# Kernel optimization log

Measured on AMD Instinct MI355X. Metric: run time of the kernel, lower is better.

Reference implementation:

```python
import jax, jax.numpy as jnp
import numpy as np

EMBED_DIM = 1024
NUM_HEADS = 16
HEAD_DIM = EMBED_DIM // NUM_HEADS


def setup_inputs() -> dict:
    key = jax.random.key(0)
    ks = jax.random.split(key, 9)
    bs, seq_len = 4, 2048
    s = 1.0 / np.sqrt(EMBED_DIM)
    return {
        "x": jax.random.normal(ks[0], (bs, seq_len, EMBED_DIM), jnp.float32),
        "wq": jax.random.uniform(ks[1], (EMBED_DIM, EMBED_DIM), jnp.float32, -s, s),
        "bq": jax.random.uniform(ks[2], (EMBED_DIM,), jnp.float32, -s, s),
        "wk": jax.random.uniform(ks[3], (EMBED_DIM, EMBED_DIM), jnp.float32, -s, s),
        "bk": jax.random.uniform(ks[4], (EMBED_DIM,), jnp.float32, -s, s),
        "wv": jax.random.uniform(ks[5], (EMBED_DIM, EMBED_DIM), jnp.float32, -s, s),
        "bv": jax.random.uniform(ks[6], (EMBED_DIM,), jnp.float32, -s, s),
        "wo": jax.random.uniform(ks[7], (EMBED_DIM, EMBED_DIM), jnp.float32, -s, s),
        "bo": jax.random.uniform(ks[8], (EMBED_DIM,), jnp.float32, -s, s),
    }


def reference(x, wq, bq, wk, bk, wv, bv, wo, bo):
    bs, seq_len, _ = x.shape
    # projections (torch Linear: y = x @ W.T + b; here w stored as [out,in])
    q = x @ wq.T + bq
    k = x @ wk.T + bk
    v = x @ wv.T + bv
    # split heads -> (bs, heads, seq, head_dim)
    def split(t):
        return t.reshape(bs, seq_len, NUM_HEADS, HEAD_DIM).transpose(0, 2, 1, 3)
    q, k, v = split(q), split(k), split(v)
    scale = 1.0 / jnp.sqrt(jnp.asarray(HEAD_DIM, jnp.float32))
    scores = jnp.einsum("bhqd,bhkd->bhqk", q, k) * scale
    attn = jax.nn.softmax(scores, axis=-1)
    out = jnp.einsum("bhqk,bhkd->bhqd", attn, v)
    out = out.transpose(0, 2, 1, 3).reshape(bs, seq_len, EMBED_DIM)
    return out @ wo.T + bo
```

## Files before the change

kernel.cpp:

```cpp
#include <hip/hip_runtime.h>
#include <stdint.h>

#define SEQ 2048
#define BSZ 4
#define NH 16
#define HD 64
#define EMB 1024
#define NT (SEQ / 64)
#define QSCALE 0.1803368801111f

using bf16x8 = __attribute__((ext_vector_type(8))) __bf16;
using u16x8  = __attribute__((ext_vector_type(8))) unsigned short;
using u32x4  = __attribute__((ext_vector_type(4))) uint32_t;
using f32x4  = __attribute__((ext_vector_type(4))) float;
using f32x16 = __attribute__((ext_vector_type(16))) float;

__device__ __forceinline__ float exp2v(float x) { return __builtin_amdgcn_exp2f(x); }

__device__ __forceinline__ unsigned short f2bf(float f) {
    union { float f; uint32_t u; } v; v.f = f;
    uint32_t r = v.u + 0x7fffu + ((v.u >> 16) & 1u);
    return (unsigned short)(r >> 16);
}

__device__ __forceinline__ uint32_t cvtpk(float lo, float hi) {
    uint32_t r;
    asm("v_cvt_pk_bf16_f32 %0, %1, %2" : "=v"(r) : "v"(lo), "v"(hi));
    return r;
}
__device__ __forceinline__ void plswap(uint32_t& a, uint32_t& b) {
    asm volatile("v_permlane32_swap_b32 %0, %1" : "+v"(a), "+v"(b));
}

__device__ __forceinline__ void gload16(void* lds, const void* g) {
    __builtin_amdgcn_global_load_lds(
        (const __attribute__((address_space(1))) void*)g,
        (__attribute__((address_space(3))) void*)lds, 16, 0, 0);
}

__global__ void cast_kernel(const float* __restrict__ s, unsigned short* __restrict__ d, int n) {
    int i = (blockIdx.x * blockDim.x + threadIdx.x) * 4;
    if (i + 3 >= n) {
        for (int j = 0; j < 4 && i + j < n; ++j) d[i + j] = f2bf(s[i + j]);
        return;
    }
    float4 v = *(const float4*)(s + i);
    ushort4 o;
    o.x = f2bf(v.x); o.y = f2bf(v.y); o.z = f2bf(v.z); o.w = f2bf(v.w);
    *(ushort4*)(d + i) = o;
}

template <int MODE>
__global__ __launch_bounds__(256, 2)
void gemm_bt(const unsigned short* __restrict__ A,
             const unsigned short* __restrict__ Bw,
             const float* __restrict__ b0, const float* __restrict__ b1,
             const float* __restrict__ b2,
             void* __restrict__ C0, void* __restrict__ C1, void* __restrict__ C2,
             int M, int N, int Kd) {
    __shared__ unsigned short As[128][64];
    __shared__ unsigned short Bs[128][64];

    const int t    = threadIdx.x;
    const int lane = t & 63;
    const int wid  = t >> 6;
    const int g    = lane >> 4;
    const int lr   = lane & 15;
    const int wm   = wid >> 1, wn = wid & 1;
    const int m0   = blockIdx.x * 128, n0 = blockIdx.y * 128;
    const int srow = lane >> 3;
    const int scol = (lane & 7) * 8;

    f32x4 acc[4][4];
    const f32x4 zero = {0.f, 0.f, 0.f, 0.f};
#pragma unroll
    for (int i = 0; i < 4; ++i)
#pragma unroll
        for (int j = 0; j < 4; ++j) acc[i][j] = zero;

    for (int kt = 0; kt < Kd; kt += 64) {
#pragma unroll
        for (int p = 0; p < 4; ++p) {
            int rowA = wid * 32 + p * 8;
            gload16(&As[rowA][0], A  + (size_t)(m0 + rowA + srow) * Kd + kt + scol);
            gload16(&Bs[rowA][0], Bw + (size_t)(n0 + rowA + srow) * Kd + kt + scol);
        }
        __syncthreads();
#pragma unroll
        for (int ks = 0; ks < 2; ++ks) {
            bf16x8 af[4], bfr[4];
#pragma unroll
            for (int m = 0; m < 4; ++m)
                af[m] = *(const bf16x8*)&As[wm * 64 + m * 16 + lr][ks * 32 + g * 8];
#pragma unroll
            for (int n = 0; n < 4; ++n)
                bfr[n] = *(const bf16x8*)&Bs[wn * 64 + n * 16 + lr][ks * 32 + g * 8];
#pragma unroll
            for (int m = 0; m < 4; ++m)
#pragma unroll
                for (int n = 0; n < 4; ++n)
                    acc[m][n] = __builtin_amdgcn_mfma_f32_16x16x32_bf16(af[m], bfr[n], acc[m][n], 0, 0, 0);
        }
        __syncthreads();
    }

    const float* bias;
    unsigned short* Cw = nullptr;
    float* Cf = nullptr;
    float scl = 1.0f;
    int nl;
    if (MODE == 2) {
        int seg = n0 >> 10;
        bias = seg == 0 ? b0 : (seg == 1 ? b1 : b2);
        Cw = (unsigned short*)(seg == 0 ? C0 : (seg == 1 ? C1 : C2));
        scl = seg == 0 ? QSCALE : 1.0f;
        nl = n0 & 1023;
    } else {
        bias = b0; Cf = (float*)C0; nl = n0;
    }
#pragma unroll
    for (int n = 0; n < 4; ++n) {
        int colL = nl + wn * 64 + n * 16 + lr;
        float bv = bias[colL];
#pragma unroll
        for (int m = 0; m < 4; ++m) {
            int rowg = m0 + wm * 64 + m * 16 + g * 4;
#pragma unroll
            for (int r = 0; r < 4; ++r) {
                float val = (acc[m][n][r] + bv) * scl;
                if (MODE == 2)
                    Cw[(size_t)(rowg + r) * EMB + colL] = f2bf(val);
                else
                    Cf[(size_t)(rowg + r) * EMB + colL] = val;
            }
        }
    }
}

template <int M>
__device__ __forceinline__ void xr(uint32_t d[4], int i) {
    uint32_t o[4];
#pragma unroll
    for (int k = 0; k < 4; ++k) o[k] = (uint32_t)__shfl_xor((int)d[k], M);
    if (M == 1) {
        bool hi = (i & 1) != 0;
#pragma unroll
        for (int k = 0; k < 4; ++k)
            d[k] = hi ? ((d[k] & 0xffff0000u) | (o[k] >> 16))
                      : ((d[k] & 0x0000ffffu) | (o[k] << 16));
    } else {
        const int mb = M >> 1;
        bool hi = (i & M) != 0;
#pragma unroll
        for (int jd = 0; jd < 4; ++jd) {
            bool jdhi = (jd & mb) != 0;
            d[jd] = (jdhi != hi) ? o[jd ^ mb] : d[jd];
        }
    }
}

__global__ __launch_bounds__(256, 2)
void flash_attn(const unsigned short* __restrict__ Q,
                const unsigned short* __restrict__ K,
                const unsigned short* __restrict__ V,
                unsigned short* __restrict__ O) {
    __shared__ unsigned char KsB[2][64 * 128];
    __shared__ unsigned char VtB[2][64 * 128];

    const int t    = threadIdx.x;
    const int wid  = t >> 6;
    const int lane = t & 63;
    const int l31  = lane & 31;
    const int hi   = lane >> 5;
    const int hi16 = hi << 4;
    const int sw   = (l31 & 7) << 4;
    const int il   = lane & 7;
    const int b    = blockIdx.z, h = blockIdx.y;
    const int qbase = blockIdx.x * 128 + wid * 32;
    const size_t rowbase = (size_t)b * SEQ;
    const unsigned short* Kh = K + rowbase * EMB + h * HD;
    const unsigned short* Vh = V + rowbase * EMB + h * HD;

    bf16x8 qf[4];
#pragma unroll
    for (int db = 0; db < 4; ++db)
        qf[db] = *(const bf16x8*)(Q + (rowbase + qbase + l31) * EMB + h * HD + db * 16 + hi * 8);

    f32x16 o0, o1;
#pragma unroll
    for (int r = 0; r < 16; ++r) { o0[r] = 0.f; o1[r] = 0.f; }
    float me = -1e30f, lsum = 0.f;

    u16x8 kreg[2], vreg[2];
    auto load_tile = [&](int kt) {
#pragma unroll
        for (int p = 0; p < 2; ++p) {
            int c = p * 256 + t;
            kreg[p] = *(const u16x8*)(Kh + (size_t)(kt * 64 + (c >> 3)) * EMB + ((c & 7) << 3));
        }
#pragma unroll
        for (int vq = 0; vq < 2; ++vq)
            vreg[vq] = *(const u16x8*)(Vh + (size_t)(kt * 64 + (vq * 4 + wid) * 8 + il) * EMB
                                          + (((lane >> 3) & 7) << 3));
    };
    load_tile(0);

    for (int kt = 0; kt < NT; ++kt) {
        unsigned char* Ks = KsB[kt & 1];
        unsigned char* Vt = VtB[kt & 1];

        uint32_t tv[2][4];
#pragma unroll
        for (int vq = 0; vq < 2; ++vq) {
            u32x4 w = __builtin_bit_cast(u32x4, vreg[vq]);
#pragma unroll
            for (int k = 0; k < 4; ++k) tv[vq][k] = w[k];
            xr<4>(tv[vq], il);
            xr<2>(tv[vq], il);
            xr<1>(tv[vq], il);
        }
#pragma unroll
        for (int p = 0; p < 2; ++p) {
            int c = p * 256 + t;
            int row = c >> 3;
            *(u16x8*)(Ks + row * 128 + ((((c & 7) << 4)) ^ ((row & 7) << 4))) = kreg[p];
        }
#pragma unroll
        for (int vq = 0; vq < 2; ++vq)
            *(u32x4*)(Vt + lane * 128 + ((((vq * 4 + wid) << 4)) ^ ((lane & 7) << 4))) = *(u32x4*)tv[vq];

        if (kt + 1 < NT) load_tile(kt + 1);

        __syncthreads();

        f32x16 s0, s1;
#pragma unroll
        for (int r = 0; r < 16; ++r) { s0[r] = 0.f; s1[r] = 0.f; }
        __builtin_amdgcn_s_setprio(1);
#pragma unroll
        for (int db = 0; db < 4; ++db) {
            bf16x8 kf0 = *(const bf16x8*)(Ks + l31 * 128        + ((db * 32 + hi16) ^ sw));
            bf16x8 kf1 = *(const bf16x8*)(Ks + (l31 + 32) * 128 + ((db * 32 + hi16) ^ sw));
            s0 = __builtin_amdgcn_mfma_f32_32x32x16_bf16(kf0, qf[db], s0, 0, 0, 0);
            s1 = __builtin_amdgcn_mfma_f32_32x32x16_bf16(kf1, qf[db], s1, 0, 0, 0);
        }
        __builtin_amdgcn_s_setprio(0);

        float pm = fmaxf(s0[0], s0[1]);
#pragma unroll
        for (int r = 2; r < 16; ++r) pm = fmaxf(pm, s0[r]);
#pragma unroll
        for (int r = 0; r < 16; ++r) pm = fmaxf(pm, s1[r]);
        pm = fmaxf(pm, __shfl_xor(pm, 32));

        if (!__all(pm - me <= 8.0f)) {
            float mn = fmaxf(me, pm);
            float al = exp2v(me - mn);
            me = mn;
            lsum *= al;
#pragma unroll
            for (int r = 0; r < 16; ++r) {
                int addr = hi16 + (((r & 3) + 8 * (r >> 2)) << 2);
                float ar = __int_as_float(
                    __builtin_amdgcn_ds_bpermute(addr, __float_as_int(al)));
                o0[r] *= ar; o1[r] *= ar;
            }
        }

        float rs = 0.f;
#pragma unroll
        for (int r = 0; r < 16; ++r) { s0[r] = exp2v(s0[r] - me); rs += s0[r]; }
#pragma unroll
        for (int r = 0; r < 16; ++r) { s1[r] = exp2v(s1[r] - me); rs += s1[r]; }
        rs += __shfl_xor(rs, 32);
        lsum += rs;

        bf16x8 pa[4];
#pragma unroll
        for (int kb = 0; kb < 2; ++kb) {
            uint32_t dw[8];
#pragma unroll
            for (int i = 0; i < 8; ++i)
                dw[i] = kb == 0 ? cvtpk(s0[2 * i], s0[2 * i + 1])
                                : cvtpk(s1[2 * i], s1[2 * i + 1]);
            plswap(dw[0], dw[2]); plswap(dw[1], dw[3]);
            plswap(dw[4], dw[6]); plswap(dw[5], dw[7]);
            u32x4 w0 = {dw[0], dw[1], dw[2], dw[3]};
            u32x4 w1 = {dw[4], dw[5], dw[6], dw[7]};
            pa[kb * 2]     = __builtin_bit_cast(bf16x8, w0);
            pa[kb * 2 + 1] = __builtin_bit_cast(bf16x8, w1);
        }

        __builtin_amdgcn_s_setprio(1);
#pragma unroll
        for (int kk = 0; kk < 4; ++kk) {
            bf16x8 vf0 = *(const bf16x8*)(Vt + l31 * 128        + ((kk * 32 + hi16) ^ sw));
            bf16x8 vf1 = *(const bf16x8*)(Vt + (l31 + 32) * 128 + ((kk * 32 + hi16) ^ sw));
            o0 = __builtin_amdgcn_mfma_f32_32x32x16_bf16(pa[kk], vf0, o0, 0, 0, 0);
            o1 = __builtin_amdgcn_mfma_f32_32x32x16_bf16(pa[kk], vf1, o1, 0, 0, 0);
        }
        __builtin_amdgcn_s_setprio(0);
    }

#pragma unroll
    for (int r = 0; r < 16; ++r) {
        int addr = hi16 + (((r & 3) + 8 * (r >> 2)) << 2);
        float lr_ = __int_as_float(__builtin_amdgcn_ds_bpermute(addr, __float_as_int(lsum)));
        float inv = 1.0f / lr_;
        int q = qbase + (r & 3) + 8 * (r >> 2) + 4 * hi;
        size_t ro = (rowbase + q) * EMB + h * HD;
        O[ro + l31]      = f2bf(o0[r] * inv);
        O[ro + 32 + l31] = f2bf(o1[r] * inv);
    }
}

extern "C" void kernel_launch(void* const* d_in, const int* in_sizes, int n_in,
                              void* d_out, int out_size, void* d_ws, size_t ws_size,
                              hipStream_t stream) {
    const float* x  = (const float*)d_in[0];
    const float* wq = (const float*)d_in[1];
    const float* bq = (const float*)d_in[2];
    const float* wk = (const float*)d_in[3];
    const float* bk = (const float*)d_in[4];
    const float* wv = (const float*)d_in[5];
    const float* bv = (const float*)d_in[6];
    const float* wo = (const float*)d_in[7];
    const float* bo = (const float*)d_in[8];

    char* ws = (char*)d_ws;
    const size_t M = (size_t)BSZ * SEQ;
    unsigned short* xb    = (unsigned short*)ws;
    unsigned short* wqkvb = (unsigned short*)(ws + (size_t)16 * 1024 * 1024);
    unsigned short* wob   = (unsigned short*)(ws + (size_t)22 * 1024 * 1024);
    unsigned short* Qb    = (unsigned short*)(ws + (size_t)24 * 1024 * 1024);
    unsigned short* Kb    = Qb + M * EMB;
    unsigned short* Vb    = Kb + M * EMB;

    const int nX = (int)(M * EMB);
    cast_kernel<<<nX / 1024, 256, 0, stream>>>(x, xb, nX);
    cast_kernel<<<1024, 256, 0, stream>>>(wq, wqkvb,                 EMB * EMB);
    cast_kernel<<<1024, 256, 0, stream>>>(wk, wqkvb + 1024 * 1024,   EMB * EMB);
    cast_kernel<<<1024, 256, 0, stream>>>(wv, wqkvb + 2 * 1024 * 1024, EMB * EMB);
    cast_kernel<<<1024, 256, 0, stream>>>(wo, wob, EMB * EMB);

    gemm_bt<2><<<dim3(64, 24), 256, 0, stream>>>(xb, wqkvb, bq, bk, bv,
                                                 Qb, Kb, Vb, (int)M, 3 * EMB, EMB);

    flash_attn<<<dim3(SEQ / 128, NH, BSZ), 256, 0, stream>>>(Qb, Kb, Vb, xb);

    gemm_bt<0><<<dim3(64, 8), 256, 0, stream>>>(xb, wob, bo, nullptr, nullptr,
                                                d_out, nullptr, nullptr, (int)M, EMB, EMB);
}
```

Before: 237.2 us.

## Double flash-attention workgroup to 8 waves and remap block IDs across XCDs

The attention kernel now runs 512 threads (8 waves) per workgroup over 256 query rows, so each K/V tile loaded into shared memory is reused by twice as many waves. Each thread loads one K and one V vector per tile instead of two. Block IDs are also permuted so that consecutive workgroups for the same head land on the same XCD, which is meant to improve L2 reuse of K/V. The trade-off is fewer workgroups, a larger synchronisation group, and launch bounds that may constrain registers.

```diff
diff --git a/kernel.cpp b/kernel.cpp
--- a/kernel.cpp
+++ b/kernel.cpp
@@ -159,13 +159,21 @@
     }
 }
 
-__global__ __launch_bounds__(256, 2)
+__global__ __launch_bounds__(512, 4)
 void flash_attn(const unsigned short* __restrict__ Q,
                 const unsigned short* __restrict__ K,
                 const unsigned short* __restrict__ V,
                 unsigned short* __restrict__ O) {
     __shared__ unsigned char KsB[2][64 * 128];
     __shared__ unsigned char VtB[2][64 * 128];
+
+    const int nwg  = gridDim.x * gridDim.y * gridDim.z;
+    const int cpx  = nwg >> 3;
+    const int bid0 = (blockIdx.z * gridDim.y + blockIdx.y) * gridDim.x + blockIdx.x;
+    const int bid  = (bid0 % 8) * cpx + (bid0 / 8);
+    const int bx   = bid & (gridDim.x - 1);
+    const int h    = (bid >> 3) & 15;
+    const int b    = bid >> 7;
 
     const int t    = threadIdx.x;
     const int wid  = t >> 6;
@@ -175,8 +183,7 @@
     const int hi16 = hi << 4;
     const int sw   = (l31 & 7) << 4;
     const int il   = lane & 7;
-    const int b    = blockIdx.z, h = blockIdx.y;
-    const int qbase = blockIdx.x * 128 + wid * 32;
+    const int qbase = bx * 256 + wid * 32;
     const size_t rowbase = (size_t)b * SEQ;
     const unsigned short* Kh = K + rowbase * EMB + h * HD;
     const unsigned short* Vh = V + rowbase * EMB + h * HD;
@@ -191,17 +198,13 @@
     for (int r = 0; r < 16; ++r) { o0[r] = 0.f; o1[r] = 0.f; }
     float me = -1e30f, lsum = 0.f;
 
-    u16x8 kreg[2], vreg[2];
+    const int krow = t >> 3;
+    const int kcol = (t & 7) << 3;
+    const int vcb  = (lane >> 3) << 3;
+    u16x8 kreg, vreg;
     auto load_tile = [&](int kt) {
-#pragma unroll
-        for (int p = 0; p < 2; ++p) {
-            int c = p * 256 + t;
-            kreg[p] = *(const u16x8*)(Kh + (size_t)(kt * 64 + (c >> 3)) * EMB + ((c & 7) << 3));
-        }
-#pragma unroll
-        for (int vq = 0; vq < 2; ++vq)
-            vreg[vq] = *(const u16x8*)(Vh + (size_t)(kt * 64 + (vq * 4 + wid) * 8 + il) * EMB
-                                          + (((lane >> 3) & 7) << 3));
+        kreg = *(const u16x8*)(Kh + (size_t)(kt * 64 + krow) * EMB + kcol);
+        vreg = *(const u16x8*)(Vh + (size_t)(kt * 64 + wid * 8 + il) * EMB + vcb);
     };
     load_tile(0);
 
@@ -209,25 +212,17 @@
         unsigned char* Ks = KsB[kt & 1];
         unsigned char* Vt = VtB[kt & 1];
 
-        uint32_t tv[2][4];
-#pragma unroll
-        for (int vq = 0; vq < 2; ++vq) {
-            u32x4 w = __builtin_bit_cast(u32x4, vreg[vq]);
-#pragma unroll
-            for (int k = 0; k < 4; ++k) tv[vq][k] = w[k];
-            xr<4>(tv[vq], il);
-            xr<2>(tv[vq], il);
-            xr<1>(tv[vq], il);
-        }
-#pragma unroll
-        for (int p = 0; p < 2; ++p) {
-            int c = p * 256 + t;
-            int row = c >> 3;
-            *(u16x8*)(Ks + row * 128 + ((((c & 7) << 4)) ^ ((row & 7) << 4))) = kreg[p];
-        }
-#pragma unroll
-        for (int vq = 0; vq < 2; ++vq)
-            *(u32x4*)(Vt + lane * 128 + ((((vq * 4 + wid) << 4)) ^ ((lane & 7) << 4))) = *(u32x4*)tv[vq];
+        uint32_t tv[4];
+        {
+            u32x4 w = __builtin_bit_cast(u32x4, vreg);
+#pragma unroll
+            for (int k = 0; k < 4; ++k) tv[k] = w[k];
+            xr<4>(tv, il);
+            xr<2>(tv, il);
+            xr<1>(tv, il);
+        }
+        *(u16x8*)(Ks + krow * 128 + (((t & 7) << 4) ^ ((krow & 7) << 4))) = kreg;
+        *(u32x4*)(Vt + lane * 128 + ((wid << 4) ^ ((lane & 7) << 4))) = *(u32x4*)tv;
 
         if (kt + 1 < NT) load_tile(kt + 1);
 
@@ -346,7 +341,7 @@
     gemm_bt<2><<<dim3(64, 24), 256, 0, stream>>>(xb, wqkvb, bq, bk, bv,
                                                  Qb, Kb, Vb, (int)M, 3 * EMB, EMB);
 
-    flash_attn<<<dim3(SEQ / 128, NH, BSZ), 256, 0, stream>>>(Qb, Kb, Vb, xb);
+    flash_attn<<<dim3(SEQ / 256, NH, BSZ), 512, 0, stream>>>(Qb, Kb, Vb, xb);
 
     gemm_bt<0><<<dim3(64, 8), 256, 0, stream>>>(xb, wob, bo, nullptr, nullptr,
                                                 d_out, nullptr, nullptr, (int)M, EMB, EMB);
```

Result: faster. 221.4 us (-6.7%).
